# Optimization experiments

Hardware: AMD Instinct MI355X
Metric: run time of the kernel (lower is better)

Reference implementation:

```python
import jax, jax.numpy as jnp
import numpy as np

N_NODES = 100000
N_EDGES = 3200000
IN_DIM, HIDDEN, OUT_DIM = 512, 128, 64


def setup_inputs() -> dict:
    key = jax.random.key(0)
    ks = jax.random.split(key, 6)
    features = jax.random.normal(ks[0], (N_NODES, IN_DIM), dtype=jnp.float32)
    W1 = jax.random.normal(ks[1], (IN_DIM, HIDDEN), dtype=jnp.float32) * (1.0 / np.sqrt(IN_DIM))
    W2 = jax.random.normal(ks[2], (HIDDEN, OUT_DIM), dtype=jnp.float32) * (1.0 / np.sqrt(HIDDEN))
    edge_weight = jax.random.uniform(ks[3], (N_EDGES,), dtype=jnp.float32)
    edge_src = jax.random.randint(ks[4], (N_EDGES,), 0, N_NODES, dtype=jnp.int32)
    edge_dst = jax.random.randint(ks[5], (N_EDGES,), 0, N_NODES, dtype=jnp.int32)
    return {"features": features, "W1": W1, "W2": W2,
            "edge_weight": edge_weight, "edge_src": edge_src, "edge_dst": edge_dst}


def _propagate(h, edge_weight, edge_src, edge_dst):
    # z = A @ h, A given as COO edge list. Equivalent to the chunked spmm:
    # Graph_output[j] = sum_i adj_chunk[i][j] @ feature_chunk[i]
    msgs = edge_weight[:, None] * h[edge_src]          # [E, D]
    return jax.ops.segment_sum(msgs, edge_dst, num_segments=N_NODES)


def reference(features, W1, W2, edge_weight, edge_src, edge_dst):
    # NN layers: mm + relu between layers, no relu after last (nlayers=2)
    h = jax.nn.relu(features @ W1)
    h = h @ W2
    # Graph propagation applied nlayers (=2) times; the feature-dim padding
    # in the torch code is a no-op on the math (stripped after the loop).
    h = _propagate(h, edge_weight, edge_src, edge_dst)
    h = _propagate(h, edge_weight, edge_src, edge_dst)
    return h
```

## Files before the change

kernel.cpp:

```cpp
#include <hip/hip_runtime.h>

#define NN    100000
#define IND   512
#define HID   128
#define OUTD  64
#define NBUCK 782
#define NB    256
#define NGEMM 782
#define NPREP 64

typedef _Float16 half8_t __attribute__((ext_vector_type(8)));
typedef _Float16 half4_t __attribute__((ext_vector_type(4)));
typedef float f32x4 __attribute__((ext_vector_type(4)));

__global__ __launch_bounds__(1024) void countprep_k(const int* __restrict__ dst,
                                                    int* __restrict__ counts, int nE, int CH,
                                                    const float* __restrict__ W1,
                                                    const float* __restrict__ W2,
                                                    _Float16* __restrict__ W1t,
                                                    _Float16* __restrict__ W2t) {
    __shared__ int bins[NBUCK];
    const int bid = blockIdx.x, tid = threadIdx.x;
    if (bid >= NB) {
        int idx = (bid - NB) * 1024 + tid;
        if (idx < IND * HID) { int c = idx >> 9, k = idx & 511; W1t[idx] = (_Float16)W1[k * HID + c]; }
        if (idx < HID * OUTD) { int c = idx >> 7, k = idx & 127; W2t[idx] = (_Float16)W2[k * OUTD + c]; }
        return;
    }
    for (int b = tid; b < NBUCK; b += 1024) bins[b] = 0;
    __syncthreads();
    const int lo = bid * CH, hi = min(lo + CH, nE);
    if (((lo | (hi - lo)) & 3) == 0) {
        for (int e = lo + tid * 4; e < hi; e += 4096) {
            int4 d = *(const int4*)(dst + e);
            atomicAdd(&bins[d.x >> 7], 1);
            atomicAdd(&bins[d.y >> 7], 1);
            atomicAdd(&bins[d.z >> 7], 1);
            atomicAdd(&bins[d.w >> 7], 1);
        }
    } else {
        for (int e = lo + tid; e < hi; e += 1024) atomicAdd(&bins[dst[e] >> 7], 1);
    }
    __syncthreads();
    for (int b = tid; b < NBUCK; b += 1024) counts[b * NB + bid] = bins[b];
}

__global__ __launch_bounds__(256) void bsum_k(const int* __restrict__ counts,
                                              int* __restrict__ bsum) {
    __shared__ int s[256];
    const int b = blockIdx.x, t = threadIdx.x;
    s[t] = counts[b * NB + t];
    __syncthreads();
    for (int off = 128; off > 0; off >>= 1) {
        if (t < off) s[t] += s[t + off];
        __syncthreads();
    }
    if (t == 0) bsum[b] = s[0];
}

__global__ __launch_bounds__(1024) void scan_top_k(const int* __restrict__ bsum,
                                                   int* __restrict__ bucketStart, int n) {
    __shared__ int s[1024];
    const int t = threadIdx.x;
    int v = (t < n) ? bsum[t] : 0;
    s[t] = v;
    __syncthreads();
    for (int off = 1; off < 1024; off <<= 1) {
        int x = (t >= off) ? s[t - off] : 0;
        __syncthreads();
        s[t] += x;
        __syncthreads();
    }
    if (t < n) bucketStart[t] = s[t] - v;
    if (t == n - 1) bucketStart[n] = s[t];
}

__global__ __launch_bounds__(256) void boff_k(int* __restrict__ counts,
                                              const int* __restrict__ bucketStart) {
    __shared__ int s[256];
    const int b = blockIdx.x, t = threadIdx.x;
    int v = counts[b * NB + t];
    s[t] = v;
    __syncthreads();
    for (int off = 1; off < 256; off <<= 1) {
        int x = (t >= off) ? s[t - off] : 0;
        __syncthreads();
        s[t] += x;
        __syncthreads();
    }
    counts[b * NB + t] = bucketStart[b] + s[t] - v;
}

__global__ __launch_bounds__(1024) void part_k(const int* __restrict__ src,
                                               const int* __restrict__ dst,
                                               const float* __restrict__ ew,
                                               const int* __restrict__ offsets,
                                               unsigned* __restrict__ edata, int nE, int CH) {
    __shared__ int cur[NBUCK];
    const int j = blockIdx.x, tid = threadIdx.x;
    for (int b = tid; b < NBUCK; b += 1024) cur[b] = offsets[b * NB + j];
    __syncthreads();
    const int lo = j * CH, hi = min(lo + CH, nE);
    if (((lo | (hi - lo)) & 3) == 0) {
        for (int e = lo + tid * 4; e < hi; e += 4096) {
            int4   d4 = *(const int4*)(dst + e);
            int4   s4 = *(const int4*)(src + e);
            float4 w4 = *(const float4*)(ew + e);
#pragma unroll
            for (int k = 0; k < 4; k++) {
                int   d = k == 0 ? d4.x : k == 1 ? d4.y : k == 2 ? d4.z : d4.w;
                int   s = k == 0 ? s4.x : k == 1 ? s4.y : k == 2 ? s4.z : s4.w;
                float w = k == 0 ? w4.x : k == 1 ? w4.y : k == 2 ? w4.z : w4.w;
                int pos = atomicAdd(&cur[d >> 7], 1);
                int q = (int)(w * 255.f + 0.5f);
                if (q > 255) q = 255;
                edata[pos] = ((unsigned)(d & 127) << 25) | ((unsigned)s << 8) | (unsigned)q;
            }
        }
    } else {
        for (int e = lo + tid; e < hi; e += 1024) {
            int d = dst[e];
            int pos = atomicAdd(&cur[d >> 7], 1);
            int q = (int)(ew[e] * 255.f + 0.5f);
            if (q > 255) q = 255;
            edata[pos] = ((unsigned)(d & 127) << 25) | ((unsigned)src[e] << 8) | (unsigned)q;
        }
    }
}

__global__ __launch_bounds__(256) void gemmsort_k(const float* __restrict__ F,
                                                  const _Float16* __restrict__ W1t,
                                                  const _Float16* __restrict__ W2t,
                                                  _Float16* __restrict__ H2,
                                                  const unsigned* __restrict__ edata,
                                                  const int* __restrict__ bucketStart,
                                                  unsigned* __restrict__ epack,
                                                  int* __restrict__ rowStart) {
    __shared__ _Float16 smem[128 * 64 * 2];
    __shared__ _Float16 W2s[64 * 128];
    const int tid = threadIdx.x;

    if (blockIdx.x < NBUCK) {
        int* bins = (int*)smem;
        int* s    = bins + 128;
        int* cur  = bins + 256;
        const int b = blockIdx.x;
        if (tid < 128) bins[tid] = 0;
        __syncthreads();
        const int beg = bucketStart[b], end = bucketStart[b + 1];
        for (int e = beg + tid; e < end; e += 256)
            atomicAdd(&bins[edata[e] >> 25], 1);
        __syncthreads();
        if (tid < 128) s[tid] = bins[tid];
        __syncthreads();
        for (int off = 1; off < 128; off <<= 1) {
            int x = 0;
            if (tid < 128 && tid >= off) x = s[tid - off];
            __syncthreads();
            if (tid < 128) s[tid] += x;
            __syncthreads();
        }
        if (tid < 128) {
            int excl = beg + s[tid] - bins[tid];
            cur[tid] = excl;
            rowStart[b * 128 + tid] = excl;
        }
        __syncthreads();
        for (int e = beg + tid; e < end; e += 256) {
            unsigned r = edata[e];
            int ld = r >> 25;
            int pos = atomicAdd(&cur[ld], 1);
            epack[pos] = r & 0x1FFFFFFu;
        }
        return;
    }

    _Float16* At = smem;
    _Float16* Bt = smem + 128 * 64;
    const int wid  = tid >> 6;
    const int lane = tid & 63;
    const int l15  = lane & 15;
    const int l4   = lane >> 4;
    const int brow = (blockIdx.x - NBUCK) * 128;

#pragma unroll
    for (int i = 0; i < 4; i++) {
        int idx = i * 256 + tid;
        int r = idx >> 4, sl = idx & 15;
        int u = (r * 128 + sl * 8) ^ ((r & 7) << 3);
        *(uint4*)(&W2s[u]) = *(const uint4*)(W2t + r * 128 + sl * 8);
    }

    f32x4 acc[2][8];
#pragma unroll
    for (int mt = 0; mt < 2; mt++)
#pragma unroll
        for (int nt = 0; nt < 8; nt++) acc[mt][nt] = (f32x4)0.f;

    for (int chunk = 0; chunk < 8; chunk++) {
        const int kc = chunk * 64;
#pragma unroll
        for (int i = 0; i < 8; i++) {
            int idx = i * 256 + tid;
            int r = idx >> 4, c4 = idx & 15;
            int gr = brow + r; if (gr >= NN) gr = NN - 1;
            float4 v = *(const float4*)(F + (size_t)gr * IND + kc + c4 * 4);
            half4_t h; h.x = (_Float16)v.x; h.y = (_Float16)v.y; h.z = (_Float16)v.z; h.w = (_Float16)v.w;
            int u = (r * 64 + c4 * 4) ^ ((r & 7) << 3);
            *(half4_t*)(&At[u]) = h;
        }
#pragma unroll
        for (int i = 0; i < 4; i++) {
            int idx = i * 256 + tid;
            int r = idx >> 3, sl = idx & 7;
            int u = (r * 64 + sl * 8) ^ ((r & 7) << 3);
            *(uint4*)(&Bt[u]) = *(const uint4*)(W1t + (size_t)r * IND + kc + sl * 8);
        }
        __syncthreads();
#pragma unroll
        for (int kk = 0; kk < 2; kk++) {
            const int kc2 = kk * 32;
            half8_t af[2];
#pragma unroll
            for (int mt = 0; mt < 2; mt++) {
                int rloc = wid * 32 + mt * 16 + l15;
                int u = (rloc * 64 + kc2 + l4 * 8) ^ ((rloc & 7) << 3);
                af[mt] = *(half8_t*)(&At[u]);
            }
#pragma unroll
            for (int nt = 0; nt < 8; nt++) {
                int cloc = nt * 16 + l15;
                int u = (cloc * 64 + kc2 + l4 * 8) ^ ((cloc & 7) << 3);
                half8_t bf = *(half8_t*)(&Bt[u]);
                acc[0][nt] = __builtin_amdgcn_mfma_f32_16x16x32_f16(af[0], bf, acc[0][nt], 0, 0, 0);
                acc[1][nt] = __builtin_amdgcn_mfma_f32_16x16x32_f16(af[1], bf, acc[1][nt], 0, 0, 0);
            }
        }
        __syncthreads();
    }

    _Float16* H1w = smem + wid * (32 * 128);
#pragma unroll
    for (int mt = 0; mt < 2; mt++)
#pragma unroll
        for (int nt = 0; nt < 8; nt++)
#pragma unroll
            for (int r = 0; r < 4; r++) {
                int rloc = mt * 16 + l4 * 4 + r;
                int col  = nt * 16 + l15;
                float v = acc[mt][nt][r];
                v = v > 0.f ? v : 0.f;
                int u = (rloc * 128 + col) ^ ((rloc & 7) << 3);
                H1w[u] = (_Float16)v;
            }

    f32x4 acc2[2][4];
#pragma unroll
    for (int mt = 0; mt < 2; mt++)
#pragma unroll
        for (int nt = 0; nt < 4; nt++) acc2[mt][nt] = (f32x4)0.f;

#pragma unroll
    for (int kk = 0; kk < 4; kk++) {
        const int kc = kk * 32;
        half8_t a2[2];
#pragma unroll
        for (int mt = 0; mt < 2; mt++) {
            int rloc = mt * 16 + l15;
            int u = (rloc * 128 + kc + l4 * 8) ^ ((rloc & 7) << 3);
            a2[mt] = *(half8_t*)(&H1w[u]);
        }
#pragma unroll
        for (int nt = 0; nt < 4; nt++) {
            int c = nt * 16 + l15;
            int u = (c * 128 + kc + l4 * 8) ^ ((c & 7) << 3);
            half8_t b2 = *(half8_t*)(&W2s[u]);
            acc2[0][nt] = __builtin_amdgcn_mfma_f32_16x16x32_f16(a2[0], b2, acc2[0][nt], 0, 0, 0);
            acc2[1][nt] = __builtin_amdgcn_mfma_f32_16x16x32_f16(a2[1], b2, acc2[1][nt], 0, 0, 0);
        }
    }
#pragma unroll
    for (int mt = 0; mt < 2; mt++)
#pragma unroll
        for (int nt = 0; nt < 4; nt++)
#pragma unroll
            for (int r = 0; r < 4; r++) {
                int grow = brow + wid * 32 + mt * 16 + l4 * 4 + r;
                if (grow < NN) H2[(size_t)grow * OUTD + nt * 16 + l15] = (_Float16)acc2[mt][nt][r];
            }
}

template <bool LAST>
__global__ __launch_bounds__(256) void pull_k(const _Float16* __restrict__ H,
                                              const unsigned* __restrict__ ep,
                                              const int* __restrict__ rowStart,
                                              _Float16* __restrict__ Zh,
                                              float* __restrict__ Zf) {
    int wv = (int)((blockIdx.x * (long)blockDim.x + threadIdx.x) >> 6);
    const int row = __builtin_amdgcn_readfirstlane(wv);
    const int lane = threadIdx.x & 63;
    if (row >= NN) return;
    const int beg = rowStart[row];
    const int end = rowStart[row + 1];
    float acc = 0.f;
    int i = beg;
    for (; i + 8 <= end; i += 8) {
        unsigned u0 = ep[i],     u1 = ep[i + 1], u2 = ep[i + 2], u3 = ep[i + 3];
        unsigned u4 = ep[i + 4], u5 = ep[i + 5], u6 = ep[i + 6], u7 = ep[i + 7];
        float h0 = (float)H[(size_t)(u0 >> 8) * OUTD + lane];
        float h1 = (float)H[(size_t)(u1 >> 8) * OUTD + lane];
        float h2 = (float)H[(size_t)(u2 >> 8) * OUTD + lane];
        float h3 = (float)H[(size_t)(u3 >> 8) * OUTD + lane];
        float h4 = (float)H[(size_t)(u4 >> 8) * OUTD + lane];
        float h5 = (float)H[(size_t)(u5 >> 8) * OUTD + lane];
        float h6 = (float)H[(size_t)(u6 >> 8) * OUTD + lane];
        float h7 = (float)H[(size_t)(u7 >> 8) * OUTD + lane];
        acc += (float)(int)(u0 & 255u) * h0;
        acc += (float)(int)(u1 & 255u) * h1;
        acc += (float)(int)(u2 & 255u) * h2;
        acc += (float)(int)(u3 & 255u) * h3;
        acc += (float)(int)(u4 & 255u) * h4;
        acc += (float)(int)(u5 & 255u) * h5;
        acc += (float)(int)(u6 & 255u) * h6;
        acc += (float)(int)(u7 & 255u) * h7;
    }
    for (; i + 4 <= end; i += 4) {
        unsigned u0 = ep[i], u1 = ep[i + 1], u2 = ep[i + 2], u3 = ep[i + 3];
        float h0 = (float)H[(size_t)(u0 >> 8) * OUTD + lane];
        float h1 = (float)H[(size_t)(u1 >> 8) * OUTD + lane];
        float h2 = (float)H[(size_t)(u2 >> 8) * OUTD + lane];
        float h3 = (float)H[(size_t)(u3 >> 8) * OUTD + lane];
        acc += (float)(int)(u0 & 255u) * h0;
        acc += (float)(int)(u1 & 255u) * h1;
        acc += (float)(int)(u2 & 255u) * h2;
        acc += (float)(int)(u3 & 255u) * h3;
    }
    for (; i < end; i++) {
        unsigned u = ep[i];
        acc += (float)(int)(u & 255u) * (float)H[(size_t)(u >> 8) * OUTD + lane];
    }
    acc *= (1.f / 255.f);
    if (LAST) Zf[(size_t)row * OUTD + lane] = acc;
    else      Zh[(size_t)row * OUTD + lane] = (_Float16)acc;
}

extern "C" void kernel_launch(void* const* d_in, const int* in_sizes, int n_in,
                              void* d_out, int out_size, void* d_ws, size_t ws_size,
                              hipStream_t stream) {
    const float* F   = (const float*)d_in[0];
    const float* W1  = (const float*)d_in[1];
    const float* W2  = (const float*)d_in[2];
    const float* ew  = (const float*)d_in[3];
    const int*   src = (const int*)d_in[4];
    const int*   dst = (const int*)d_in[5];
    float* out = (float*)d_out;
    const int nE = in_sizes[3];

    char* p = (char*)d_ws;
    _Float16*  h2        = (_Float16*)p;  p += (size_t)NN * OUTD * sizeof(_Float16);
    _Float16*  z1        = (_Float16*)p;  p += (size_t)NN * OUTD * sizeof(_Float16);
    _Float16*  W1t       = (_Float16*)p;  p += (size_t)HID * IND * sizeof(_Float16);
    _Float16*  W2t       = (_Float16*)p;  p += (size_t)OUTD * HID * sizeof(_Float16);
    int*       counts    = (int*)p;       p += (size_t)NBUCK * NB * sizeof(int);
    int*       bsum      = (int*)p;       p += (size_t)NBUCK * sizeof(int);
    int*       bucketStart=(int*)p;       p += (size_t)(NBUCK + 16) * sizeof(int);
    int*       rowStart  = (int*)p;       p += (size_t)(NN + 160) * sizeof(int);
    unsigned*  edata     = (unsigned*)p;  p += (size_t)nE * sizeof(unsigned);
    unsigned*  epack     = (unsigned*)p;  p += (size_t)nE * sizeof(unsigned);

    const int CH = (nE + NB - 1) / NB;

    countprep_k<<<NB + NPREP, 1024, 0, stream>>>(dst, counts, nE, CH, W1, W2, W1t, W2t);
    bsum_k<<<NBUCK, 256, 0, stream>>>(counts, bsum);
    scan_top_k<<<1, 1024, 0, stream>>>(bsum, bucketStart, NBUCK);
    boff_k<<<NBUCK, 256, 0, stream>>>(counts, bucketStart);
    part_k<<<NB, 1024, 0, stream>>>(src, dst, ew, counts, edata, nE, CH);

    gemmsort_k<<<NBUCK + NGEMM, 256, 0, stream>>>(F, W1t, W2t, h2,
                                                  edata, bucketStart, epack, rowStart);

    int blocks = (int)(((long)NN * 64 + 255) / 256);
    pull_k<false><<<blocks, 256, 0, stream>>>(h2, epack, rowStart, z1, nullptr);
    pull_k<true><<<blocks, 256, 0, stream>>>(z1, epack, rowStart, nullptr, out);
}
```

Before: 249.0 us.

## Load GEMM tiles directly into LDS with global_load_lds and pre-swizzled W1

The first-layer GEMM now streams fp32 feature tiles and a pre-swizzled fp16 W1 straight from global memory into LDS using global_load_lds. This bypasses the register round trip and the per-element fp32-to-fp16 conversion at store time; conversion now happens when fragments are read from LDS. The K chunk is halved to 32 so the fp32 tile fits in LDS, and W1 is reloaded only every other chunk. The trade-off is twice as many barriers, and the fp32 A tile takes more LDS space and LDS read bandwidth.

New measurement: 249.1 us. No clear change (+0.0%).

```diff
diff --git a/kernel.cpp b/kernel.cpp
--- a/kernel.cpp
+++ b/kernel.cpp
@@ -9,6 +9,9 @@
 #define NGEMM 782
 #define NPREP 64
 
+#define AS1 __attribute__((address_space(1)))
+#define AS3 __attribute__((address_space(3)))
+
 typedef _Float16 half8_t __attribute__((ext_vector_type(8)));
 typedef _Float16 half4_t __attribute__((ext_vector_type(4)));
 typedef float f32x4 __attribute__((ext_vector_type(4)));
@@ -17,13 +20,17 @@
                                                     int* __restrict__ counts, int nE, int CH,
                                                     const float* __restrict__ W1,
                                                     const float* __restrict__ W2,
-                                                    _Float16* __restrict__ W1t,
+                                                    _Float16* __restrict__ W1s,
                                                     _Float16* __restrict__ W2t) {
     __shared__ int bins[NBUCK];
     const int bid = blockIdx.x, tid = threadIdx.x;
     if (bid >= NB) {
         int idx = (bid - NB) * 1024 + tid;
-        if (idx < IND * HID) { int c = idx >> 9, k = idx & 511; W1t[idx] = (_Float16)W1[k * HID + c]; }
+        if (idx < IND * HID) {
+            int c = idx >> 9, k = idx & 511;
+            int dk = (k & ~63) | ((k & 63) ^ ((c & 7) << 3));
+            W1s[c * 512 + dk] = (_Float16)W1[k * HID + c];
+        }
         if (idx < HID * OUTD) { int c = idx >> 7, k = idx & 127; W2t[idx] = (_Float16)W2[k * OUTD + c]; }
         return;
     }
@@ -129,15 +136,17 @@
 }
 
 __global__ __launch_bounds__(256) void gemmsort_k(const float* __restrict__ F,
-                                                  const _Float16* __restrict__ W1t,
+                                                  const _Float16* __restrict__ W1s,
                                                   const _Float16* __restrict__ W2t,
                                                   _Float16* __restrict__ H2,
                                                   const unsigned* __restrict__ edata,
                                                   const int* __restrict__ bucketStart,
                                                   unsigned* __restrict__ epack,
                                                   int* __restrict__ rowStart) {
-    __shared__ _Float16 smem[128 * 64 * 2];
-    __shared__ _Float16 W2s[64 * 128];
+    __shared__ char smem[49152];
+    float*     Af32 = (float*)smem;
+    _Float16*  Btb  = (_Float16*)(smem + 16384);
+    _Float16*  W2s  = (_Float16*)(smem + 32768);
     const int tid = threadIdx.x;
 
     if (blockIdx.x < NBUCK) {
@@ -175,13 +184,12 @@
         return;
     }
 
-    _Float16* At = smem;
-    _Float16* Bt = smem + 128 * 64;
     const int wid  = tid >> 6;
     const int lane = tid & 63;
     const int l15  = lane & 15;
     const int l4   = lane >> 4;
     const int brow = (blockIdx.x - NBUCK) * 128;
+    const int wlds = (tid >> 6) * 1024;
 
 #pragma unroll
     for (int i = 0; i < 4; i++) {
@@ -197,49 +205,59 @@
 #pragma unroll
         for (int nt = 0; nt < 8; nt++) acc[mt][nt] = (f32x4)0.f;
 
-    for (int chunk = 0; chunk < 8; chunk++) {
-        const int kc = chunk * 64;
-#pragma unroll
-        for (int i = 0; i < 8; i++) {
-            int idx = i * 256 + tid;
-            int r = idx >> 4, c4 = idx & 15;
+    for (int chunk = 0; chunk < 16; chunk++) {
+        const int kc = chunk * 32;
+#pragma unroll
+        for (int i = 0; i < 4; i++) {
+            int Lb = i * 4096 + tid * 16;
+            int r  = Lb >> 7;
+            int ls = ((Lb >> 4) & 7) ^ (r & 7);
             int gr = brow + r; if (gr >= NN) gr = NN - 1;
-            float4 v = *(const float4*)(F + (size_t)gr * IND + kc + c4 * 4);
-            half4_t h; h.x = (_Float16)v.x; h.y = (_Float16)v.y; h.z = (_Float16)v.z; h.w = (_Float16)v.w;
-            int u = (r * 64 + c4 * 4) ^ ((r & 7) << 3);
-            *(half4_t*)(&At[u]) = h;
-        }
-#pragma unroll
-        for (int i = 0; i < 4; i++) {
-            int idx = i * 256 + tid;
-            int r = idx >> 3, sl = idx & 7;
-            int u = (r * 64 + sl * 8) ^ ((r & 7) << 3);
-            *(uint4*)(&Bt[u]) = *(const uint4*)(W1t + (size_t)r * IND + kc + sl * 8);
-        }
-        __syncthreads();
-#pragma unroll
-        for (int kk = 0; kk < 2; kk++) {
-            const int kc2 = kk * 32;
-            half8_t af[2];
-#pragma unroll
-            for (int mt = 0; mt < 2; mt++) {
-                int rloc = wid * 32 + mt * 16 + l15;
-                int u = (rloc * 64 + kc2 + l4 * 8) ^ ((rloc & 7) << 3);
-                af[mt] = *(half8_t*)(&At[u]);
+            const float* gp = F + (size_t)gr * IND + kc + ls * 4;
+            __builtin_amdgcn_global_load_lds((const AS1 void*)gp,
+                (AS3 void*)(smem + i * 4096 + wlds), 16, 0, 0);
+        }
+        if ((chunk & 1) == 0) {
+#pragma unroll
+            for (int i = 0; i < 4; i++) {
+                int Lb = i * 4096 + tid * 16;
+                int eo = Lb >> 1;
+                int r  = eo >> 6;
+                int c6 = eo & 63;
+                const _Float16* gp = W1s + (size_t)r * IND + (chunk >> 1) * 64 + c6;
+                __builtin_amdgcn_global_load_lds((const AS1 void*)gp,
+                    (AS3 void*)(smem + 16384 + i * 4096 + wlds), 16, 0, 0);
             }
-#pragma unroll
-            for (int nt = 0; nt < 8; nt++) {
-                int cloc = nt * 16 + l15;
-                int u = (cloc * 64 + kc2 + l4 * 8) ^ ((cloc & 7) << 3);
-                half8_t bf = *(half8_t*)(&Bt[u]);
-                acc[0][nt] = __builtin_amdgcn_mfma_f32_16x16x32_f16(af[0], bf, acc[0][nt], 0, 0, 0);
-                acc[1][nt] = __builtin_amdgcn_mfma_f32_16x16x32_f16(af[1], bf, acc[1][nt], 0, 0, 0);
-            }
-        }
-        __syncthreads();
-    }
-
-    _Float16* H1w = smem + wid * (32 * 128);
+        }
+        __syncthreads();
+
+        half8_t af[2];
+#pragma unroll
+        for (int mt = 0; mt < 2; mt++) {
+            int rl = wid * 32 + mt * 16 + l15;
+            int s0 = l4 * 2;
+            f32x4 a0 = *(f32x4*)((char*)Af32 + rl * 128 + (((s0    ) ^ (rl & 7)) << 4));
+            f32x4 a1 = *(f32x4*)((char*)Af32 + rl * 128 + (((s0 + 1) ^ (rl & 7)) << 4));
+            half8_t h;
+            h[0] = (_Float16)a0[0]; h[1] = (_Float16)a0[1];
+            h[2] = (_Float16)a0[2]; h[3] = (_Float16)a0[3];
+            h[4] = (_Float16)a1[0]; h[5] = (_Float16)a1[1];
+            h[6] = (_Float16)a1[2]; h[7] = (_Float16)a1[3];
+            af[mt] = h;
+        }
+        const int kc2l = (chunk & 1) * 32;
+#pragma unroll
+        for (int nt = 0; nt < 8; nt++) {
+            int cl = nt * 16 + l15;
+            int u = (cl * 64 + kc2l + l4 * 8) ^ ((cl & 7) << 3);
+            half8_t bf = *(half8_t*)(&Btb[u]);
+            acc[0][nt] = __builtin_amdgcn_mfma_f32_16x16x32_f16(af[0], bf, acc[0][nt], 0, 0, 0);
+            acc[1][nt] = __builtin_amdgcn_mfma_f32_16x16x32_f16(af[1], bf, acc[1][nt], 0, 0, 0);
+        }
+        __syncthreads();
+    }
+
+    _Float16* H1w = (_Float16*)smem + wid * (32 * 128);
 #pragma unroll
     for (int mt = 0; mt < 2; mt++)
 #pragma unroll
@@ -359,7 +377,7 @@
     char* p = (char*)d_ws;
     _Float16*  h2        = (_Float16*)p;  p += (size_t)NN * OUTD * sizeof(_Float16);
     _Float16*  z1        = (_Float16*)p;  p += (size_t)NN * OUTD * sizeof(_Float16);
-    _Float16*  W1t       = (_Float16*)p;  p += (size_t)HID * IND * sizeof(_Float16);
+    _Float16*  W1s       = (_Float16*)p;  p += (size_t)HID * IND * sizeof(_Float16);
     _Float16*  W2t       = (_Float16*)p;  p += (size_t)OUTD * HID * sizeof(_Float16);
     int*       counts    = (int*)p;       p += (size_t)NBUCK * NB * sizeof(int);
     int*       bsum      = (int*)p;       p += (size_t)NBUCK * sizeof(int);
@@ -370,13 +388,13 @@
 
     const int CH = (nE + NB - 1) / NB;
 
-    countprep_k<<<NB + NPREP, 1024, 0, stream>>>(dst, counts, nE, CH, W1, W2, W1t, W2t);
+    countprep_k<<<NB + NPREP, 1024, 0, stream>>>(dst, counts, nE, CH, W1, W2, W1s, W2t);
     bsum_k<<<NBUCK, 256, 0, stream>>>(counts, bsum);
     scan_top_k<<<1, 1024, 0, stream>>>(bsum, bucketStart, NBUCK);
     boff_k<<<NBUCK, 256, 0, stream>>>(counts, bucketStart);
     part_k<<<NB, 1024, 0, stream>>>(src, dst, ew, counts, edata, nE, CH);
 
-    gemmsort_k<<<NBUCK + NGEMM, 256, 0, stream>>>(F, W1t, W2t, h2,
+    gemmsort_k<<<NBUCK + NGEMM, 256, 0, stream>>>(F, W1s, W2t, h2,
                                                   edata, bucketStart, epack, rowStart);
 
     int blocks = (int)(((long)NN * 64 + 255) / 256);
```
